# Kernel optimization log

Measured on AMD Instinct MI355X. Metric: run time of the kernel, lower is better.

The kernel has to match this reference:

```python
import jax, jax.numpy as jnp
import numpy as np

D, N_EXP, TOP_K = 2048, 64, 8
B, S = 4, 4096

def setup_inputs() -> dict:
    key = jax.random.key(0)
    k1, k2, k3, k4 = jax.random.split(key, 4)
    hidden_states = jax.random.normal(k1, (B, S, D), dtype=jnp.float32)
    # nn.Linear weights are [out, in]; default init ~ U(-1/sqrt(d), 1/sqrt(d))
    bound = 1.0 / np.sqrt(D)
    W_gate = jax.random.uniform(k2, (N_EXP, D), jnp.float32, -bound, bound)
    W_noise = 0.01 * jax.random.normal(k3, (N_EXP, D), dtype=jnp.float32)
    # training-mode noise (router_step % top_k == 0 path): fixed-seed randn
    noise = jax.random.normal(k4, (B, S, N_EXP), dtype=jnp.float32)
    return {"hidden_states": hidden_states, "W_gate": W_gate,
            "W_noise": W_noise, "noise": noise}

def reference(hidden_states, W_gate, W_noise, noise):
    # logits = h @ W_gate^T  : [B,S,n_exp]
    logits = jnp.einsum('bsd,ed->bse', hidden_states, W_gate)
    scale = jax.nn.softplus(jnp.einsum('bsd,ed->bse', hidden_states, W_noise))
    logits = logits + noise * scale
    gates = jax.nn.softmax(logits, axis=-1)
    vals, inds = jax.lax.top_k(gates, TOP_K)  # sorted desc (torch used sorted=False)
    return vals, inds, gates
```

## Files before the change

kernel.cpp:

```cpp
#include <hip/hip_runtime.h>
#include <math.h>

typedef __attribute__((ext_vector_type(8))) _Float16 half8;
typedef __attribute__((ext_vector_type(4))) float    f32x4;

constexpr int D_DIM = 2048;
constexpr int NEXP  = 64;
constexpr int TOPK  = 8;
constexpr int NTOK  = 16384;
constexpr int TM    = 64;
constexpr int BK    = 32;
constexpr int NCH   = D_DIM / BK;
constexpr int OSTR  = 132;
constexpr int NSTR  = 68;
constexpr float WSCALE   = 4096.0f;
constexpr float INV_WSC  = 1.0f / 4096.0f;

__device__ __forceinline__ unsigned short f16b(float x) {
    _Float16 h = (_Float16)x;
    return __builtin_bit_cast(unsigned short, h);
}
__device__ __forceinline__ float f16tof(unsigned short b) {
    return (float)__builtin_bit_cast(_Float16, b);
}

__global__ void prep_w(const float* __restrict__ Wg, const float* __restrict__ Wn,
                       unsigned short* __restrict__ wsB)
{
    const int idx = blockIdx.x * blockDim.x + threadIdx.x;
    const int n   = idx >> 8;
    const int K8  = idx & 255;
    const float* src = (n < 64) ? (Wg + (size_t)n * D_DIM)
                                : (Wn + (size_t)(n - 64) * D_DIM);
    float4 a = *reinterpret_cast<const float4*>(src + K8 * 8);
    float4 b = *reinterpret_cast<const float4*>(src + K8 * 8 + 4);

    float v[8] = {a.x, a.y, a.z, a.w, b.x, b.y, b.z, b.w};
    union { unsigned short u[8]; half8 s; } H, L;
#pragma unroll
    for (int j = 0; j < 8; ++j) {
        float xs = v[j] * WSCALE;
        unsigned short h = f16b(xs);
        H.u[j] = h;
        L.u[j] = f16b(xs - f16tof(h));
    }
    const int l = ((K8 & 3) * 16) + (n & 15);
    const size_t base = (size_t)(K8 >> 2) * 8192 + (size_t)(n >> 4) * 1024 + (size_t)l * 8;
    *reinterpret_cast<half8*>(wsB + base)       = H.s;
    *reinterpret_cast<half8*>(wsB + base + 512) = L.s;
}

__global__ __launch_bounds__(512, 1)
void noisy_topk_router(const float* __restrict__ hs,
                       const unsigned short* __restrict__ wsB,
                       const float* __restrict__ nz,
                       float* __restrict__ out)
{
    __shared__ __align__(16) char smem[33792 + 17408];
    unsigned short* stage  = reinterpret_cast<unsigned short*>(smem);
    float*          logits = reinterpret_cast<float*>(smem);
    float*          ldsN   = reinterpret_cast<float*>(smem + 33792);

    const int tid  = threadIdx.x;
    const int lane = tid & 63;
    const int w    = tid >> 6;
    const int t0   = blockIdx.x * TM;

    const int tok_s = tid >> 3;
    const int g2    = tid & 7;
    const int mrow  = tok_s & 15;
    const int mtile = tok_s >> 4;
    const int g     = g2 >> 1;
    const int half  = g2 & 1;
    const float* hrow = hs + (size_t)(t0 + tok_s) * D_DIM + g2 * 4;
    const int wr_hi = mtile * 512 + (g * 16 + mrow) * 8 + half * 4;

    f32x4 accH0[4], accH1[4], accX[4];
#pragma unroll
    for (int mt = 0; mt < 4; ++mt) {
        accH0[mt] = (f32x4){0.f, 0.f, 0.f, 0.f};
        accH1[mt] = (f32x4){0.f, 0.f, 0.f, 0.f};
        accX[mt]  = (f32x4){0.f, 0.f, 0.f, 0.f};
    }

    auto cvt_write = [&](float4 v, unsigned short* buf) {
        float p[4] = {v.x, v.y, v.z, v.w};
        unsigned int Hp[2], Lp[2];
#pragma unroll
        for (int q = 0; q < 2; ++q) {
            unsigned short h0 = f16b(p[2*q]);
            unsigned short h1 = f16b(p[2*q+1]);
            unsigned short l0 = f16b(p[2*q]   - f16tof(h0));
            unsigned short l1 = f16b(p[2*q+1] - f16tof(h1));
            Hp[q] = (unsigned int)h0 | ((unsigned int)h1 << 16);
            Lp[q] = (unsigned int)l0 | ((unsigned int)l1 << 16);
        }
        *reinterpret_cast<uint2*>(buf + wr_hi)        = make_uint2(Hp[0], Hp[1]);
        *reinterpret_cast<uint2*>(buf + 2048 + wr_hi) = make_uint2(Lp[0], Lp[1]);
    };

    cvt_write(*reinterpret_cast<const float4*>(hrow), stage);
    float4 pf_cur = *reinterpret_cast<const float4*>(hrow + BK);
    __syncthreads();

    const unsigned short* bp0 = wsB + (size_t)w * 1024 + (size_t)lane * 8;

    auto kstep = [&](int c, f32x4* accH) {
        const int buf = c & 1;
        float4 pf_next;
        if (c + 2 < NCH)
            pf_next = *reinterpret_cast<const float4*>(hrow + (c + 2) * BK);

        const unsigned short* bp = bp0 + (size_t)c * 8192;
        half8 bhi = *reinterpret_cast<const half8*>(bp);
        half8 blo = *reinterpret_cast<const half8*>(bp + 512);

        const unsigned short* sb = stage + buf * 4096;
        half8 ahi[4], alo[4];
#pragma unroll
        for (int mt = 0; mt < 4; ++mt) {
            ahi[mt] = *reinterpret_cast<const half8*>(sb + mt * 512 + lane * 8);
            alo[mt] = *reinterpret_cast<const half8*>(sb + 2048 + mt * 512 + lane * 8);
        }

#pragma unroll
        for (int mt = 0; mt < 4; ++mt) {
            accH[mt] = __builtin_amdgcn_mfma_f32_16x16x32_f16(ahi[mt], bhi, accH[mt], 0, 0, 0);
            accX[mt] = __builtin_amdgcn_mfma_f32_16x16x32_f16(ahi[mt], blo, accX[mt], 0, 0, 0);
            accX[mt] = __builtin_amdgcn_mfma_f32_16x16x32_f16(alo[mt], bhi, accX[mt], 0, 0, 0);
        }

        if (c + 1 < NCH) {
            cvt_write(pf_cur, stage + (buf ^ 1) * 4096);
            pf_cur = pf_next;
        }
        __syncthreads();
    };

    for (int c2 = 0; c2 < NCH; c2 += 2) {
        kstep(c2,     accH0);
        kstep(c2 + 1, accH1);
    }

    {
        const int colb = w * 16 + (lane & 15);
        const int rowb = (lane >> 4) * 4;
#pragma unroll
        for (int mt = 0; mt < 4; ++mt) {
            f32x4 s = accH0[mt] + accH1[mt] + accX[mt];
#pragma unroll
            for (int r = 0; r < 4; ++r)
                logits[(mt * 16 + rowb + r) * OSTR + colb] = s[r] * INV_WSC;
        }
    }
    {
        const int rr = tid >> 3;
        const int cc = tid & 7;
        const float* nrow = nz + (size_t)(t0 + rr) * NEXP;
#pragma unroll
        for (int p = 0; p < 2; ++p) {
            float4 v = *reinterpret_cast<const float4*>(nrow + cc * 4 + p * 32);
            *reinterpret_cast<float4*>(&ldsN[rr * NSTR + cc * 4 + p * 32]) = v;
        }
    }
    __syncthreads();

    if (tid < TM) {
        const int tok = t0 + tid;
        float l[NEXP];
        float mx = -3.0e38f;
#pragma unroll
        for (int e = 0; e < NEXP; ++e) {
            float gsc = logits[tid * OSTR + e];
            float nl  = logits[tid * OSTR + 64 + e];
            float sp  = fmaxf(nl, 0.0f) + log1pf(expf(-fabsf(nl)));
            float le  = fmaf(ldsN[tid * NSTR + e], sp, gsc);
            l[e] = le;
            mx = fmaxf(mx, le);
        }
        float sum = 0.0f;
#pragma unroll
        for (int e = 0; e < NEXP; ++e) { float p = expf(l[e] - mx); l[e] = p; sum += p; }
        float inv = 1.0f / sum;
#pragma unroll
        for (int e = 0; e < NEXP; ++e) l[e] *= inv;

#pragma unroll
        for (int e = 0; e < NEXP; ++e) logits[tid * OSTR + e] = l[e];

        float* vout = out + (size_t)tok * TOPK;
        float* iout = out + (size_t)NTOK * TOPK + (size_t)tok * TOPK;
#pragma unroll
        for (int p = 0; p < TOPK; ++p) {
            float m = -1.0f; int mi = 0;
#pragma unroll
            for (int e = 0; e < NEXP; ++e) {
                bool gt = l[e] > m;
                m  = gt ? l[e] : m;
                mi = gt ? e : mi;
            }
            vout[p] = m;
            iout[p] = (float)mi;
#pragma unroll
            for (int e = 0; e < NEXP; ++e) l[e] = (e == mi) ? -1.0f : l[e];
        }
    }
    __syncthreads();

    {
        const int rr = tid >> 3;
        const int cc = tid & 7;
        float* gout = out + (size_t)NTOK * TOPK * 2;
#pragma unroll
        for (int p = 0; p < 2; ++p) {
            float4 v = *reinterpret_cast<const float4*>(&logits[rr * OSTR + cc * 4 + p * 32]);
            *reinterpret_cast<float4*>(&gout[(size_t)(t0 + rr) * NEXP + cc * 4 + p * 32]) = v;
        }
    }
}

extern "C" void kernel_launch(void* const* d_in, const int* in_sizes, int n_in,
                              void* d_out, int out_size, void* d_ws, size_t ws_size,
                              hipStream_t stream) {
    const float* hs = (const float*)d_in[0];
    const float* Wg = (const float*)d_in[1];
    const float* Wn = (const float*)d_in[2];
    const float* nz = (const float*)d_in[3];
    float* out = (float*)d_out;
    unsigned short* wsB = (unsigned short*)d_ws;

    prep_w<<<64, 512, 0, stream>>>(Wg, Wn, wsB);
    noisy_topk_router<<<NTOK / TM, 512, 0, stream>>>(hs, wsB, nz, out);
}
```

Measured before the change: 264.4 us.

## Split K across wave halves and load activations directly into registers

Replaces the LDS-staged activation pipeline, which needed a barrier every K-chunk, with per-wave direct global loads. Each lane converts its own fp32 activations into hi/lo fp16 MFMA fragments in registers. Waves are split into two K-halves, each covering 32 output columns with register double-buffered prefetch, and the halves are reduced through LDS at the end. This removes the per-step syncthreads and LDS round trip. In exchange, each wave loads activations redundantly from global memory and register pressure rises with 16 accumulators plus prefetch buffers.

Result: slower. 281.3 us (+6.4%).

```diff
diff --git a/kernel.cpp b/kernel.cpp
--- a/kernel.cpp
+++ b/kernel.cpp
@@ -9,12 +9,10 @@
 constexpr int TOPK  = 8;
 constexpr int NTOK  = 16384;
 constexpr int TM    = 64;
-constexpr int BK    = 32;
-constexpr int NCH   = D_DIM / BK;
 constexpr int OSTR  = 132;
 constexpr int NSTR  = 68;
-constexpr float WSCALE   = 4096.0f;
-constexpr float INV_WSC  = 1.0f / 4096.0f;
+constexpr float WSCALE  = 4096.0f;
+constexpr float INV_WSC = 1.0f / 4096.0f;
 
 __device__ __forceinline__ unsigned short f16b(float x) {
     _Float16 h = (_Float16)x;
@@ -56,102 +54,122 @@
                        const float* __restrict__ nz,
                        float* __restrict__ out)
 {
-    __shared__ __align__(16) char smem[33792 + 17408];
-    unsigned short* stage  = reinterpret_cast<unsigned short*>(smem);
-    float*          logits = reinterpret_cast<float*>(smem);
-    float*          ldsN   = reinterpret_cast<float*>(smem + 33792);
+    __shared__ float logits[TM * OSTR];
+    __shared__ float ldsN[TM * NSTR];
 
     const int tid  = threadIdx.x;
     const int lane = tid & 63;
     const int w    = tid >> 6;
     const int t0   = blockIdx.x * TM;
-
-    const int tok_s = tid >> 3;
-    const int g2    = tid & 7;
-    const int mrow  = tok_s & 15;
-    const int mtile = tok_s >> 4;
-    const int g     = g2 >> 1;
-    const int half  = g2 & 1;
-    const float* hrow = hs + (size_t)(t0 + tok_s) * D_DIM + g2 * 4;
-    const int wr_hi = mtile * 512 + (g * 16 + mrow) * 8 + half * 4;
-
-    f32x4 accH0[4], accH1[4], accX[4];
+    const int kh   = w >> 2;
+    const int wp   = w & 3;
+
+    const float* abase = hs + (size_t)(t0 + (lane & 15)) * D_DIM + kh * 1024 + ((lane >> 4) * 8);
+    const unsigned short* bbase = wsB + (size_t)(kh * 32) * 8192 + (size_t)(2 * wp) * 1024 + (size_t)lane * 8;
+
+    f32x4 accH[4][2], accX[4][2];
+#pragma unroll
+    for (int mt = 0; mt < 4; ++mt)
+#pragma unroll
+        for (int ntk = 0; ntk < 2; ++ntk) {
+            accH[mt][ntk] = (f32x4){0.f, 0.f, 0.f, 0.f};
+            accX[mt][ntk] = (f32x4){0.f, 0.f, 0.f, 0.f};
+        }
+
+    float4 curA[4][2];
+    uint4  curB[2][2];
 #pragma unroll
     for (int mt = 0; mt < 4; ++mt) {
-        accH0[mt] = (f32x4){0.f, 0.f, 0.f, 0.f};
-        accH1[mt] = (f32x4){0.f, 0.f, 0.f, 0.f};
-        accX[mt]  = (f32x4){0.f, 0.f, 0.f, 0.f};
-    }
-
-    auto cvt_write = [&](float4 v, unsigned short* buf) {
-        float p[4] = {v.x, v.y, v.z, v.w};
-        unsigned int Hp[2], Lp[2];
-#pragma unroll
-        for (int q = 0; q < 2; ++q) {
-            unsigned short h0 = f16b(p[2*q]);
-            unsigned short h1 = f16b(p[2*q+1]);
-            unsigned short l0 = f16b(p[2*q]   - f16tof(h0));
-            unsigned short l1 = f16b(p[2*q+1] - f16tof(h1));
-            Hp[q] = (unsigned int)h0 | ((unsigned int)h1 << 16);
-            Lp[q] = (unsigned int)l0 | ((unsigned int)l1 << 16);
-        }
-        *reinterpret_cast<uint2*>(buf + wr_hi)        = make_uint2(Hp[0], Hp[1]);
-        *reinterpret_cast<uint2*>(buf + 2048 + wr_hi) = make_uint2(Lp[0], Lp[1]);
-    };
-
-    cvt_write(*reinterpret_cast<const float4*>(hrow), stage);
-    float4 pf_cur = *reinterpret_cast<const float4*>(hrow + BK);
+        const float* p = abase + (size_t)mt * (16 * D_DIM);
+        curA[mt][0] = *reinterpret_cast<const float4*>(p);
+        curA[mt][1] = *reinterpret_cast<const float4*>(p + 4);
+    }
+#pragma unroll
+    for (int ntk = 0; ntk < 2; ++ntk) {
+        const unsigned short* p = bbase + ntk * 1024;
+        curB[ntk][0] = *reinterpret_cast<const uint4*>(p);
+        curB[ntk][1] = *reinterpret_cast<const uint4*>(p + 512);
+    }
+
+#pragma unroll 2
+    for (int c = 0; c < 32; ++c) {
+        const int cn = (c + 1 < 32) ? (c + 1) : 31;
+
+        float4 nA[4][2];
+        uint4  nB[2][2];
+#pragma unroll
+        for (int mt = 0; mt < 4; ++mt) {
+            const float* p = abase + (size_t)mt * (16 * D_DIM) + cn * 32;
+            nA[mt][0] = *reinterpret_cast<const float4*>(p);
+            nA[mt][1] = *reinterpret_cast<const float4*>(p + 4);
+        }
+#pragma unroll
+        for (int ntk = 0; ntk < 2; ++ntk) {
+            const unsigned short* p = bbase + (size_t)cn * 8192 + ntk * 1024;
+            nB[ntk][0] = *reinterpret_cast<const uint4*>(p);
+            nB[ntk][1] = *reinterpret_cast<const uint4*>(p + 512);
+        }
+
+        half8 ahi[4], alo[4];
+#pragma unroll
+        for (int mt = 0; mt < 4; ++mt) {
+            float x[8] = {curA[mt][0].x, curA[mt][0].y, curA[mt][0].z, curA[mt][0].w,
+                          curA[mt][1].x, curA[mt][1].y, curA[mt][1].z, curA[mt][1].w};
+            union { unsigned short u[8]; half8 v; } H, L;
+#pragma unroll
+            for (int j = 0; j < 8; ++j) {
+                unsigned short h = f16b(x[j]);
+                H.u[j] = h;
+                L.u[j] = f16b(x[j] - f16tof(h));
+            }
+            ahi[mt] = H.v;
+            alo[mt] = L.v;
+        }
+        half8 bhi[2], blo[2];
+#pragma unroll
+        for (int ntk = 0; ntk < 2; ++ntk) {
+            bhi[ntk] = __builtin_bit_cast(half8, curB[ntk][0]);
+            blo[ntk] = __builtin_bit_cast(half8, curB[ntk][1]);
+        }
+
+#pragma unroll
+        for (int mt = 0; mt < 4; ++mt)
+#pragma unroll
+            for (int ntk = 0; ntk < 2; ++ntk) {
+                accH[mt][ntk] = __builtin_amdgcn_mfma_f32_16x16x32_f16(ahi[mt], bhi[ntk], accH[mt][ntk], 0, 0, 0);
+                accX[mt][ntk] = __builtin_amdgcn_mfma_f32_16x16x32_f16(ahi[mt], blo[ntk], accX[mt][ntk], 0, 0, 0);
+                accX[mt][ntk] = __builtin_amdgcn_mfma_f32_16x16x32_f16(alo[mt], bhi[ntk], accX[mt][ntk], 0, 0, 0);
+            }
+
+#pragma unroll
+        for (int mt = 0; mt < 4; ++mt) { curA[mt][0] = nA[mt][0]; curA[mt][1] = nA[mt][1]; }
+#pragma unroll
+        for (int ntk = 0; ntk < 2; ++ntk) { curB[ntk][0] = nB[ntk][0]; curB[ntk][1] = nB[ntk][1]; }
+    }
+
+    const int colb = 2 * wp * 16 + (lane & 15);
+    const int rowb = (lane >> 4) * 4;
+    if (w >= 4) {
+#pragma unroll
+        for (int mt = 0; mt < 4; ++mt)
+#pragma unroll
+            for (int ntk = 0; ntk < 2; ++ntk)
+#pragma unroll
+                for (int r = 0; r < 4; ++r)
+                    logits[(mt * 16 + rowb + r) * OSTR + colb + ntk * 16] =
+                        accH[mt][ntk][r] + accX[mt][ntk][r];
+    }
     __syncthreads();
-
-    const unsigned short* bp0 = wsB + (size_t)w * 1024 + (size_t)lane * 8;
-
-    auto kstep = [&](int c, f32x4* accH) {
-        const int buf = c & 1;
-        float4 pf_next;
-        if (c + 2 < NCH)
-            pf_next = *reinterpret_cast<const float4*>(hrow + (c + 2) * BK);
-
-        const unsigned short* bp = bp0 + (size_t)c * 8192;
-        half8 bhi = *reinterpret_cast<const half8*>(bp);
-        half8 blo = *reinterpret_cast<const half8*>(bp + 512);
-
-        const unsigned short* sb = stage + buf * 4096;
-        half8 ahi[4], alo[4];
-#pragma unroll
-        for (int mt = 0; mt < 4; ++mt) {
-            ahi[mt] = *reinterpret_cast<const half8*>(sb + mt * 512 + lane * 8);
-            alo[mt] = *reinterpret_cast<const half8*>(sb + 2048 + mt * 512 + lane * 8);
-        }
-
-#pragma unroll
-        for (int mt = 0; mt < 4; ++mt) {
-            accH[mt] = __builtin_amdgcn_mfma_f32_16x16x32_f16(ahi[mt], bhi, accH[mt], 0, 0, 0);
-            accX[mt] = __builtin_amdgcn_mfma_f32_16x16x32_f16(ahi[mt], blo, accX[mt], 0, 0, 0);
-            accX[mt] = __builtin_amdgcn_mfma_f32_16x16x32_f16(alo[mt], bhi, accX[mt], 0, 0, 0);
-        }
-
-        if (c + 1 < NCH) {
-            cvt_write(pf_cur, stage + (buf ^ 1) * 4096);
-            pf_cur = pf_next;
-        }
-        __syncthreads();
-    };
-
-    for (int c2 = 0; c2 < NCH; c2 += 2) {
-        kstep(c2,     accH0);
-        kstep(c2 + 1, accH1);
-    }
-
-    {
-        const int colb = w * 16 + (lane & 15);
-        const int rowb = (lane >> 4) * 4;
-#pragma unroll
-        for (int mt = 0; mt < 4; ++mt) {
-            f32x4 s = accH0[mt] + accH1[mt] + accX[mt];
-#pragma unroll
-            for (int r = 0; r < 4; ++r)
-                logits[(mt * 16 + rowb + r) * OSTR + colb] = s[r] * INV_WSC;
-        }
+    if (w < 4) {
+#pragma unroll
+        for (int mt = 0; mt < 4; ++mt)
+#pragma unroll
+            for (int ntk = 0; ntk < 2; ++ntk)
+#pragma unroll
+                for (int r = 0; r < 4; ++r) {
+                    const int idx = (mt * 16 + rowb + r) * OSTR + colb + ntk * 16;
+                    logits[idx] = (logits[idx] + accH[mt][ntk][r] + accX[mt][ntk][r]) * INV_WSC;
+                }
     }
     {
         const int rr = tid >> 3;
```

## Halve token tile, double K chunk, raise occupancy to four blocks per CU

Applied to the files above, without the earlier changes.

Shrinks each block to 32 tokens and 64-wide K chunks, restructures staging layout and MFMA loop for two K sub-steps per chunk, and sets launch bounds to allow four blocks per CU with smaller LDS. Doubles the grid (512 blocks) to improve latency hiding on the memory-bound hidden-state stream. In exchange, each block re-reads the full weight matrix for fewer tokens, doubling weight traffic, and the softmax/topk tail now runs on only 32 threads per block.

Result: faster. 243.8 us (-7.8%).

```diff
diff --git a/kernel.cpp b/kernel.cpp
--- a/kernel.cpp
+++ b/kernel.cpp
@@ -8,13 +8,13 @@
 constexpr int NEXP  = 64;
 constexpr int TOPK  = 8;
 constexpr int NTOK  = 16384;
-constexpr int TM    = 64;
-constexpr int BK    = 32;
+constexpr int TM    = 32;
+constexpr int BK    = 64;
 constexpr int NCH   = D_DIM / BK;
 constexpr int OSTR  = 132;
 constexpr int NSTR  = 68;
-constexpr float WSCALE   = 4096.0f;
-constexpr float INV_WSC  = 1.0f / 4096.0f;
+constexpr float WSCALE  = 4096.0f;
+constexpr float INV_WSC = 1.0f / 4096.0f;
 
 __device__ __forceinline__ unsigned short f16b(float x) {
     _Float16 h = (_Float16)x;
@@ -50,34 +50,36 @@
     *reinterpret_cast<half8*>(wsB + base + 512) = L.s;
 }
 
-__global__ __launch_bounds__(512, 1)
+__global__ __launch_bounds__(512, 4)
 void noisy_topk_router(const float* __restrict__ hs,
                        const unsigned short* __restrict__ wsB,
                        const float* __restrict__ nz,
                        float* __restrict__ out)
 {
-    __shared__ __align__(16) char smem[33792 + 17408];
+    __shared__ __align__(16) char smem[16896 + 8704];
     unsigned short* stage  = reinterpret_cast<unsigned short*>(smem);
     float*          logits = reinterpret_cast<float*>(smem);
-    float*          ldsN   = reinterpret_cast<float*>(smem + 33792);
+    float*          ldsN   = reinterpret_cast<float*>(smem + 16896);
 
     const int tid  = threadIdx.x;
     const int lane = tid & 63;
     const int w    = tid >> 6;
     const int t0   = blockIdx.x * TM;
 
-    const int tok_s = tid >> 3;
-    const int g2    = tid & 7;
-    const int mrow  = tok_s & 15;
-    const int mtile = tok_s >> 4;
-    const int g     = g2 >> 1;
-    const int half  = g2 & 1;
-    const float* hrow = hs + (size_t)(t0 + tok_s) * D_DIM + g2 * 4;
-    const int wr_hi = mtile * 512 + (g * 16 + mrow) * 8 + half * 4;
-
-    f32x4 accH0[4], accH1[4], accX[4];
-#pragma unroll
-    for (int mt = 0; mt < 4; ++mt) {
+    const int r  = tid >> 4;
+    const int k4 = (tid & 15) * 4;
+    const float* hrow = hs + (size_t)(t0 + r) * D_DIM + k4;
+    const int ks_s = k4 >> 5;
+    const int kk   = k4 & 31;
+    const int j0   = kk >> 3;
+    const int pos  = kk & 7;
+    const int mt_s = r >> 4;
+    const int m_s  = r & 15;
+    const int wroff = (mt_s * 2 + ks_s) * 512 + (j0 * 16 + m_s) * 8 + pos;
+
+    f32x4 accH0[2], accH1[2], accX[2];
+#pragma unroll
+    for (int mt = 0; mt < 2; ++mt) {
         accH0[mt] = (f32x4){0.f, 0.f, 0.f, 0.f};
         accH1[mt] = (f32x4){0.f, 0.f, 0.f, 0.f};
         accX[mt]  = (f32x4){0.f, 0.f, 0.f, 0.f};
@@ -95,73 +97,59 @@
             Hp[q] = (unsigned int)h0 | ((unsigned int)h1 << 16);
             Lp[q] = (unsigned int)l0 | ((unsigned int)l1 << 16);
         }
-        *reinterpret_cast<uint2*>(buf + wr_hi)        = make_uint2(Hp[0], Hp[1]);
-        *reinterpret_cast<uint2*>(buf + 2048 + wr_hi) = make_uint2(Lp[0], Lp[1]);
+        *reinterpret_cast<uint2*>(buf + wroff)        = make_uint2(Hp[0], Hp[1]);
+        *reinterpret_cast<uint2*>(buf + 2048 + wroff) = make_uint2(Lp[0], Lp[1]);
     };
 
     cvt_write(*reinterpret_cast<const float4*>(hrow), stage);
-    float4 pf_cur = *reinterpret_cast<const float4*>(hrow + BK);
     __syncthreads();
 
-    const unsigned short* bp0 = wsB + (size_t)w * 1024 + (size_t)lane * 8;
-
-    auto kstep = [&](int c, f32x4* accH) {
-        const int buf = c & 1;
-        float4 pf_next;
-        if (c + 2 < NCH)
-            pf_next = *reinterpret_cast<const float4*>(hrow + (c + 2) * BK);
-
-        const unsigned short* bp = bp0 + (size_t)c * 8192;
-        half8 bhi = *reinterpret_cast<const half8*>(bp);
-        half8 blo = *reinterpret_cast<const half8*>(bp + 512);
-
-        const unsigned short* sb = stage + buf * 4096;
-        half8 ahi[4], alo[4];
-#pragma unroll
-        for (int mt = 0; mt < 4; ++mt) {
-            ahi[mt] = *reinterpret_cast<const half8*>(sb + mt * 512 + lane * 8);
-            alo[mt] = *reinterpret_cast<const half8*>(sb + 2048 + mt * 512 + lane * 8);
-        }
-
-#pragma unroll
-        for (int mt = 0; mt < 4; ++mt) {
-            accH[mt] = __builtin_amdgcn_mfma_f32_16x16x32_f16(ahi[mt], bhi, accH[mt], 0, 0, 0);
-            accX[mt] = __builtin_amdgcn_mfma_f32_16x16x32_f16(ahi[mt], blo, accX[mt], 0, 0, 0);
-            accX[mt] = __builtin_amdgcn_mfma_f32_16x16x32_f16(alo[mt], bhi, accX[mt], 0, 0, 0);
-        }
-
-        if (c + 1 < NCH) {
-            cvt_write(pf_cur, stage + (buf ^ 1) * 4096);
-            pf_cur = pf_next;
-        }
+    for (int c = 0; c < NCH; ++c) {
+        float4 pf;
+        if (c + 1 < NCH)
+            pf = *reinterpret_cast<const float4*>(hrow + (c + 1) * BK);
+
+        const unsigned short* sb = stage + (c & 1) * 4096;
+
+#pragma unroll
+        for (int ks = 0; ks < 2; ++ks) {
+            const unsigned short* bp = wsB + (size_t)(2 * c + ks) * 8192
+                                           + (size_t)w * 1024 + (size_t)lane * 8;
+            half8 bhi = *reinterpret_cast<const half8*>(bp);
+            half8 blo = *reinterpret_cast<const half8*>(bp + 512);
+#pragma unroll
+            for (int mt = 0; mt < 2; ++mt) {
+                half8 ahi = *reinterpret_cast<const half8*>(sb + (mt * 2 + ks) * 512 + lane * 8);
+                half8 alo = *reinterpret_cast<const half8*>(sb + 2048 + (mt * 2 + ks) * 512 + lane * 8);
+                if (ks == 0)
+                    accH0[mt] = __builtin_amdgcn_mfma_f32_16x16x32_f16(ahi, bhi, accH0[mt], 0, 0, 0);
+                else
+                    accH1[mt] = __builtin_amdgcn_mfma_f32_16x16x32_f16(ahi, bhi, accH1[mt], 0, 0, 0);
+                accX[mt] = __builtin_amdgcn_mfma_f32_16x16x32_f16(ahi, blo, accX[mt], 0, 0, 0);
+                accX[mt] = __builtin_amdgcn_mfma_f32_16x16x32_f16(alo, bhi, accX[mt], 0, 0, 0);
+            }
+        }
+
+        if (c + 1 < NCH)
+            cvt_write(pf, stage + ((c + 1) & 1) * 4096);
         __syncthreads();
-    };
-
-    for (int c2 = 0; c2 < NCH; c2 += 2) {
-        kstep(c2,     accH0);
-        kstep(c2 + 1, accH1);
     }
 
     {
         const int colb = w * 16 + (lane & 15);
         const int rowb = (lane >> 4) * 4;
 #pragma unroll
-        for (int mt = 0; mt < 4; ++mt) {
-            f32x4 s = accH0[mt] + accH1[mt] + accX[mt];
-#pragma unroll
-            for (int r = 0; r < 4; ++r)
-                logits[(mt * 16 + rowb + r) * OSTR + colb] = s[r] * INV_WSC;
-        }
+        for (int mt = 0; mt < 2; ++mt)
+#pragma unroll
+            for (int rr = 0; rr < 4; ++rr)
+                logits[(mt * 16 + rowb + rr) * OSTR + colb] =
+                    (accH0[mt][rr] + accH1[mt][rr] + accX[mt][rr]) * INV_WSC;
     }
     {
-        const int rr = tid >> 3;
-        const int cc = tid & 7;
-        const float* nrow = nz + (size_t)(t0 + rr) * NEXP;
-#pragma unroll
-        for (int p = 0; p < 2; ++p) {
-            float4 v = *reinterpret_cast<const float4*>(nrow + cc * 4 + p * 32);
-            *reinterpret_cast<float4*>(&ldsN[rr * NSTR + cc * 4 + p * 32]) = v;
-        }
+        const int rr = tid >> 4;
+        const int cc = tid & 15;
+        float4 v = *reinterpret_cast<const float4*>(nz + (size_t)(t0 + rr) * NEXP + cc * 4);
+        *reinterpret_cast<float4*>(&ldsN[rr * NSTR + cc * 4]) = v;
     }
     __syncthreads();
 
@@ -208,14 +196,11 @@
     __syncthreads();
 
     {
-        const int rr = tid >> 3;
-        const int cc = tid & 7;
+        const int rr = tid >> 4;
+        const int cc = tid & 15;
         float* gout = out + (size_t)NTOK * TOPK * 2;
-#pragma unroll
-        for (int p = 0; p < 2; ++p) {
-            float4 v = *reinterpret_cast<const float4*>(&logits[rr * OSTR + cc * 4 + p * 32]);
-            *reinterpret_cast<float4*>(&gout[(size_t)(t0 + rr) * NEXP + cc * 4 + p * 32]) = v;
-        }
+        float4 v = *reinterpret_cast<const float4*>(&logits[rr * OSTR + cc * 4]);
+        *reinterpret_cast<float4*>(&gout[(size_t)(t0 + rr) * NEXP + cc * 4]) = v;
     }
 }
 
```

## Stage A and B tiles via async global-to-LDS DMA with 2x2 warp tiling

Applied to the files above, without the earlier changes.

Replaces the register prefetch plus convert-then-store path for hidden states with async global_load_lds copies of raw fp32 A and pre-split fp16 B tiles into double-buffered LDS. The hi/lo fp16 split of A now happens after the LDS read, inside the k-loop. Warps are re-tiled into a 2x2 (M x N) grid of 16x16 tiles, and the weight workspace layout is changed to match. This is meant to take global load latency and VGPR staging off the critical path. In exchange, every warp redoes the A conversion for its own tiles, and one barrier per k-step now guards the async copies with no explicit wait on them.

After: 301.1 us. +13.9%, slower.

```diff
diff --git a/kernel.cpp b/kernel.cpp
--- a/kernel.cpp
+++ b/kernel.cpp
@@ -13,8 +13,8 @@
 constexpr int NCH   = D_DIM / BK;
 constexpr int OSTR  = 132;
 constexpr int NSTR  = 68;
-constexpr float WSCALE   = 4096.0f;
-constexpr float INV_WSC  = 1.0f / 4096.0f;
+constexpr float WSCALE  = 4096.0f;
+constexpr float INV_WSC = 1.0f / 4096.0f;
 
 __device__ __forceinline__ unsigned short f16b(float x) {
     _Float16 h = (_Float16)x;
@@ -22,6 +22,12 @@
 }
 __device__ __forceinline__ float f16tof(unsigned short b) {
     return (float)__builtin_bit_cast(_Float16, b);
+}
+
+__device__ __forceinline__ void async_cp16(const void* g, void* l) {
+    __builtin_amdgcn_global_load_lds(
+        (const __attribute__((address_space(1))) unsigned int*)g,
+        (__attribute__((address_space(3))) unsigned int*)l, 16, 0, 0);
 }
 
 __global__ void prep_w(const float* __restrict__ Wg, const float* __restrict__ Wn,
@@ -44,10 +50,12 @@
         H.u[j] = h;
         L.u[j] = f16b(xs - f16tof(h));
     }
-    const int l = ((K8 & 3) * 16) + (n & 15);
-    const size_t base = (size_t)(K8 >> 2) * 8192 + (size_t)(n >> 4) * 1024 + (size_t)l * 8;
-    *reinterpret_cast<half8*>(wsB + base)       = H.s;
-    *reinterpret_cast<half8*>(wsB + base + 512) = L.s;
+    const int c  = K8 >> 2;
+    const int l  = ((K8 & 3) * 16) + (n & 15);
+    const int nt = n >> 4;
+    const size_t base = (size_t)c * 8192 + (size_t)nt * 512 + (size_t)l * 8;
+    *reinterpret_cast<half8*>(wsB + base)        = H.s;
+    *reinterpret_cast<half8*>(wsB + base + 4096) = L.s;
 }
 
 __global__ __launch_bounds__(512, 1)
@@ -56,8 +64,7 @@
                        const float* __restrict__ nz,
                        float* __restrict__ out)
 {
-    __shared__ __align__(16) char smem[33792 + 17408];
-    unsigned short* stage  = reinterpret_cast<unsigned short*>(smem);
+    __shared__ __align__(16) char smem[51200];
     float*          logits = reinterpret_cast<float*>(smem);
     float*          ldsN   = reinterpret_cast<float*>(smem + 33792);
 
@@ -65,92 +72,100 @@
     const int lane = tid & 63;
     const int w    = tid >> 6;
     const int t0   = blockIdx.x * TM;
-
-    const int tok_s = tid >> 3;
-    const int g2    = tid & 7;
-    const int mrow  = tok_s & 15;
-    const int mtile = tok_s >> 4;
-    const int g     = g2 >> 1;
-    const int half  = g2 & 1;
-    const float* hrow = hs + (size_t)(t0 + tok_s) * D_DIM + g2 * 4;
-    const int wr_hi = mtile * 512 + (g * 16 + mrow) * 8 + half * 4;
-
-    f32x4 accH0[4], accH1[4], accX[4];
-#pragma unroll
-    for (int mt = 0; mt < 4; ++mt) {
-        accH0[mt] = (f32x4){0.f, 0.f, 0.f, 0.f};
-        accH1[mt] = (f32x4){0.f, 0.f, 0.f, 0.f};
-        accX[mt]  = (f32x4){0.f, 0.f, 0.f, 0.f};
-    }
-
-    auto cvt_write = [&](float4 v, unsigned short* buf) {
-        float p[4] = {v.x, v.y, v.z, v.w};
-        unsigned int Hp[2], Lp[2];
-#pragma unroll
-        for (int q = 0; q < 2; ++q) {
-            unsigned short h0 = f16b(p[2*q]);
-            unsigned short h1 = f16b(p[2*q+1]);
-            unsigned short l0 = f16b(p[2*q]   - f16tof(h0));
-            unsigned short l1 = f16b(p[2*q+1] - f16tof(h1));
-            Hp[q] = (unsigned int)h0 | ((unsigned int)h1 << 16);
-            Lp[q] = (unsigned int)l0 | ((unsigned int)l1 << 16);
-        }
-        *reinterpret_cast<uint2*>(buf + wr_hi)        = make_uint2(Hp[0], Hp[1]);
-        *reinterpret_cast<uint2*>(buf + 2048 + wr_hi) = make_uint2(Lp[0], Lp[1]);
+    const int mh   = w >> 2;
+    const int nq   = w & 3;
+    const int w4   = w - 4;
+
+    const float* aptr0 = hs + (size_t)(t0 + (lane >> 1)) * D_DIM      + w * 8 + (lane & 1) * 4;
+    const float* aptr1 = hs + (size_t)(t0 + 32 + (lane >> 1)) * D_DIM + w * 8 + (lane & 1) * 4;
+    const unsigned short* bptr = wsB + (size_t)(w4 & 3) * 2048 + (size_t)lane * 8;
+
+    auto issue_dma = [&](int c, int buf) {
+        if (w < 4) {
+            char* ad = smem + buf * 8192 + w * 2048;
+            async_cp16(aptr0 + c * BK, ad);
+            async_cp16(aptr1 + c * BK, ad + 1024);
+        } else {
+            const unsigned short* bs = bptr + (size_t)c * 8192;
+            char* bd = smem + 16384 + buf * 16384 + w4 * 4096;
+            async_cp16(bs,        bd);
+            async_cp16(bs + 512,  bd + 1024);
+            async_cp16(bs + 1024, bd + 2048);
+            async_cp16(bs + 1536, bd + 3072);
+        }
     };
 
-    cvt_write(*reinterpret_cast<const float4*>(hrow), stage);
-    float4 pf_cur = *reinterpret_cast<const float4*>(hrow + BK);
+    f32x4 accH[2][2], accX[2][2];
+#pragma unroll
+    for (int i = 0; i < 2; ++i)
+#pragma unroll
+        for (int j = 0; j < 2; ++j) {
+            accH[i][j] = (f32x4){0.f, 0.f, 0.f, 0.f};
+            accX[i][j] = (f32x4){0.f, 0.f, 0.f, 0.f};
+        }
+
+    issue_dma(0, 0);
     __syncthreads();
 
-    const unsigned short* bp0 = wsB + (size_t)w * 1024 + (size_t)lane * 8;
-
-    auto kstep = [&](int c, f32x4* accH) {
+    for (int c = 0; c < NCH; ++c) {
         const int buf = c & 1;
-        float4 pf_next;
-        if (c + 2 < NCH)
-            pf_next = *reinterpret_cast<const float4*>(hrow + (c + 2) * BK);
-
-        const unsigned short* bp = bp0 + (size_t)c * 8192;
-        half8 bhi = *reinterpret_cast<const half8*>(bp);
-        half8 blo = *reinterpret_cast<const half8*>(bp + 512);
-
-        const unsigned short* sb = stage + buf * 4096;
-        half8 ahi[4], alo[4];
-#pragma unroll
-        for (int mt = 0; mt < 4; ++mt) {
-            ahi[mt] = *reinterpret_cast<const half8*>(sb + mt * 512 + lane * 8);
-            alo[mt] = *reinterpret_cast<const half8*>(sb + 2048 + mt * 512 + lane * 8);
-        }
-
-#pragma unroll
-        for (int mt = 0; mt < 4; ++mt) {
-            accH[mt] = __builtin_amdgcn_mfma_f32_16x16x32_f16(ahi[mt], bhi, accH[mt], 0, 0, 0);
-            accX[mt] = __builtin_amdgcn_mfma_f32_16x16x32_f16(ahi[mt], blo, accX[mt], 0, 0, 0);
-            accX[mt] = __builtin_amdgcn_mfma_f32_16x16x32_f16(alo[mt], bhi, accX[mt], 0, 0, 0);
-        }
-
-        if (c + 1 < NCH) {
-            cvt_write(pf_cur, stage + (buf ^ 1) * 4096);
-            pf_cur = pf_next;
-        }
+        if (c + 1 < NCH)
+            issue_dma(c + 1, buf ^ 1);
+
+        const float*          ab = reinterpret_cast<const float*>(smem) + buf * 2048;
+        const unsigned short* bb = reinterpret_cast<const unsigned short*>(smem + 16384) + buf * 8192;
+
+        half8 ahi[2], alo[2], bhi[2], blo[2];
+#pragma unroll
+        for (int i = 0; i < 2; ++i) {
+            const int mt = mh * 2 + i;
+            const float* ap = ab + (lane >> 4) * 512 + (mt * 16 + (lane & 15)) * 8;
+            float4 x0 = *reinterpret_cast<const float4*>(ap);
+            float4 x1 = *reinterpret_cast<const float4*>(ap + 4);
+            float xx[8] = {x0.x, x0.y, x0.z, x0.w, x1.x, x1.y, x1.z, x1.w};
+            union { unsigned short u[8]; half8 v; } H, L;
+#pragma unroll
+            for (int j = 0; j < 8; ++j) {
+                unsigned short h = f16b(xx[j]);
+                H.u[j] = h;
+                L.u[j] = f16b(xx[j] - f16tof(h));
+            }
+            ahi[i] = H.v;
+            alo[i] = L.v;
+        }
+#pragma unroll
+        for (int i = 0; i < 2; ++i) {
+            const int nt = nq * 2 + i;
+            bhi[i] = *reinterpret_cast<const half8*>(bb + nt * 512 + lane * 8);
+            blo[i] = *reinterpret_cast<const half8*>(bb + 4096 + nt * 512 + lane * 8);
+        }
+
+#pragma unroll
+        for (int i = 0; i < 2; ++i)
+#pragma unroll
+            for (int j = 0; j < 2; ++j) {
+                accH[i][j] = __builtin_amdgcn_mfma_f32_16x16x32_f16(ahi[i], bhi[j], accH[i][j], 0, 0, 0);
+                accX[i][j] = __builtin_amdgcn_mfma_f32_16x16x32_f16(ahi[i], blo[j], accX[i][j], 0, 0, 0);
+                accX[i][j] = __builtin_amdgcn_mfma_f32_16x16x32_f16(alo[i], bhi[j], accX[i][j], 0, 0, 0);
+            }
+
         __syncthreads();
-    };
-
-    for (int c2 = 0; c2 < NCH; c2 += 2) {
-        kstep(c2,     accH0);
-        kstep(c2 + 1, accH1);
     }
 
     {
-        const int colb = w * 16 + (lane & 15);
-        const int rowb = (lane >> 4) * 4;
-#pragma unroll
-        for (int mt = 0; mt < 4; ++mt) {
-            f32x4 s = accH0[mt] + accH1[mt] + accX[mt];
-#pragma unroll
-            for (int r = 0; r < 4; ++r)
-                logits[(mt * 16 + rowb + r) * OSTR + colb] = s[r] * INV_WSC;
+        const int rowq = (lane >> 4) * 4;
+        const int colw = lane & 15;
+#pragma unroll
+        for (int i = 0; i < 2; ++i) {
+            const int mt = mh * 2 + i;
+#pragma unroll
+            for (int j = 0; j < 2; ++j) {
+                const int nt = nq * 2 + j;
+#pragma unroll
+                for (int r = 0; r < 4; ++r)
+                    logits[(mt * 16 + rowq + r) * OSTR + nt * 16 + colw] =
+                        (accH[i][j][r] + accX[i][j][r]) * INV_WSC;
+            }
         }
     }
     {
```
